# Optimization experiments

Measured on AMD Instinct MI355X. Metric: run time of the kernel, lower is better.

Reference implementation:

```python
import jax, jax.numpy as jnp
import numpy as np

NUM_SECTORS = 11


def setup_inputs() -> dict:
    key = jax.random.key(0)
    k0, k1, k2, k3 = jax.random.split(key, 4)
    B, N, C, H = 4, 2048, 512, 8
    x = jax.random.normal(k0, (B, N, C), dtype=jnp.float32)
    w_qkv = jax.random.normal(k1, (C, 3 * C), dtype=jnp.float32) * 0.02
    w_proj = jax.random.normal(k2, (C, C), dtype=jnp.float32) * 0.02
    b_proj = jnp.zeros((C,), dtype=jnp.float32)
    gate_logit = jnp.full((H,), 2.0, dtype=jnp.float32)
    sector_ids = jax.random.randint(k3, (N,), 0, NUM_SECTORS, dtype=jnp.int64)
    return {"x": x, "w_qkv": w_qkv, "w_proj": w_proj, "b_proj": b_proj,
            "gate_logit": gate_logit, "sector_ids": sector_ids}


def reference(x, w_qkv, w_proj, b_proj, gate_logit, sector_ids):
    B, N, C = x.shape
    H = gate_logit.shape[0]
    d = C // H
    scale = d ** -0.5

    qkv = (x @ w_qkv).reshape(B, N, 3, H, d)
    qkv = jnp.transpose(qkv, (2, 0, 3, 1, 4))  # (3, B, H, N, d)
    q, k, v = qkv[0], qkv[1], qkv[2]

    # Content attention: softmax(QK^T / sqrt(d)) @ V
    attn = jnp.einsum('bhnd,bhmd->bhnm', q, k) * scale
    attn = jax.nn.softmax(attn, axis=-1)
    v_content = jnp.einsum('bhnm,bhmd->bhnd', attn, v)

    # Positional path: A_pos @ V == per-sector mean of V, gathered per row.
    # A_pos[i,j] = 1/|sector(i)| if sector(i)==sector(j); row_sum >= 1 always.
    ids = sector_ids.astype(jnp.int32)
    counts = jax.ops.segment_sum(jnp.ones((N,), x.dtype), ids, num_segments=NUM_SECTORS)
    counts = jnp.maximum(counts, 1.0)
    v_nfirst = jnp.transpose(v, (2, 0, 1, 3)).reshape(N, B * H * d)  # (N, BHd)
    sums = jax.ops.segment_sum(v_nfirst, ids, num_segments=NUM_SECTORS)  # (S, BHd)
    means = sums / counts[:, None]
    v_pos = means[ids].reshape(N, B, H, d).transpose(1, 2, 0, 3)  # (B, H, N, d)

    g = jax.nn.sigmoid(gate_logit)[None, :, None, None]
    out = g * v_pos + (1.0 - g) * v_content  # (B, H, N, d)
    out = jnp.transpose(out, (0, 2, 1, 3)).reshape(B, N, C)
    return out @ w_proj + b_proj
```

## Files before the change

### kernel.cpp

```cpp
#include <hip/hip_runtime.h>
#include <hip/hip_bf16.h>
#include <stdint.h>

typedef float f32x4 __attribute__((ext_vector_type(4)));
typedef float f32x16 __attribute__((ext_vector_type(16)));
typedef short bf16x8 __attribute__((ext_vector_type(8)));
typedef short short4v __attribute__((ext_vector_type(4)));
typedef int i32x4 __attribute__((ext_vector_type(4)));

#define MFMA16(a, b, c) __builtin_amdgcn_mfma_f32_16x16x32_bf16(a, b, c, 0, 0, 0)
#define MFMA32(a, b, c) __builtin_amdgcn_mfma_f32_32x32x16_bf16(a, b, c, 0, 0, 0)

__device__ __forceinline__ float bf2f(unsigned short u) {
    unsigned int x = ((unsigned int)u) << 16;
    float f;
    __builtin_memcpy(&f, &x, 4);
    return f;
}
__device__ __forceinline__ unsigned short f2bf(float f) {
    unsigned int x;
    __builtin_memcpy(&x, &f, 4);
    unsigned int r = x + 0x7FFFu + ((x >> 16) & 1u);
    return (unsigned short)(r >> 16);
}
__device__ __forceinline__ unsigned int cvt_pk_bf16(float lo, float hi) {
    unsigned int d;
    asm("v_cvt_pk_bf16_f32 %0, %1, %2" : "=v"(d) : "v"(lo), "v"(hi));
    return d;
}

#define GLD16(g, l)                                                        \
    __builtin_amdgcn_global_load_lds(                                      \
        (const __attribute__((address_space(1))) void*)(g),                \
        (__attribute__((address_space(3))) void*)(l), 16, 0, 0)

#define QSCALE 0.18033688011112042f

__global__ __launch_bounds__(256) void k_cvt_x(const float* __restrict__ x,
                                               unsigned short* __restrict__ xb) {
    int i = (blockIdx.x * 256 + threadIdx.x) * 4;
    float4 v = *(const float4*)(x + i);
    short4v o;
    o.x = (short)f2bf(v.x);
    o.y = (short)f2bf(v.y);
    o.z = (short)f2bf(v.z);
    o.w = (short)f2bf(v.w);
    *(short4v*)(xb + i) = o;
}

__global__ __launch_bounds__(256) void k_transpose_bf16(const float* __restrict__ in,
                                                        unsigned short* __restrict__ out,
                                                        int R, int C) {
    __shared__ float tile[32][33];
    int tx = threadIdx.x & 31, ty = threadIdx.x >> 5;
    int r0 = blockIdx.y * 32, c0 = blockIdx.x * 32;
#pragma unroll
    for (int i = 0; i < 32; i += 8) tile[ty + i][tx] = in[(r0 + ty + i) * C + c0 + tx];
    __syncthreads();
#pragma unroll
    for (int i = 0; i < 32; i += 8) out[(c0 + ty + i) * R + r0 + tx] = f2bf(tile[tx][ty + i]);
}

__global__ __launch_bounds__(256) void k_gemm_qkv(const unsigned short* __restrict__ A,
                                                  const unsigned short* __restrict__ Bt,
                                                  unsigned short* __restrict__ Q,
                                                  unsigned short* __restrict__ Kd,
                                                  unsigned short* __restrict__ Vr) {
    __shared__ alignas(16) unsigned short As[128 * 64];
    __shared__ alignas(16) unsigned short Bs[128 * 64];
    const int t = threadIdx.x;
    const int w = t >> 6, l = t & 63;
    const int brow = blockIdx.x * 128, bcol = blockIdx.y * 128;
    const int wr = (w >> 1) * 64, wc = (w & 1) * 64;
    const int li = l & 15, lk = (l >> 4) * 8;
    f32x4 acc[4][4] = {};

    for (int kt = 0; kt < 512; kt += 64) {
#pragma unroll
        for (int i = 0; i < 4; i++) {
            int ub = i * 256 + w * 64;
            int r = (ub >> 3) + (l >> 3);
            int ck = l & 7;
            GLD16(A + (brow + r) * 512 + kt + ck * 8, As + ub * 8);
            GLD16(Bt + (bcol + r) * 512 + kt + ck * 8, Bs + ub * 8);
        }
        __syncthreads();
#pragma unroll
        for (int ks = 0; ks < 2; ks++) {
            bf16x8 af[4], bfr[4];
#pragma unroll
            for (int m = 0; m < 4; m++)
                af[m] = *(const bf16x8*)(As + (wr + m * 16 + li) * 64 + ks * 32 + lk);
#pragma unroll
            for (int n = 0; n < 4; n++)
                bfr[n] = *(const bf16x8*)(Bs + (wc + n * 16 + li) * 64 + ks * 32 + lk);
#pragma unroll
            for (int m = 0; m < 4; m++)
#pragma unroll
                for (int n = 0; n < 4; n++)
                    acc[m][n] = MFMA16(af[m], bfr[n], acc[m][n]);
        }
        __syncthreads();
    }
#pragma unroll
    for (int m = 0; m < 4; m++) {
#pragma unroll
        for (int n = 0; n < 4; n++) {
#pragma unroll
            for (int r = 0; r < 4; r++) {
                int gm = brow + wr + m * 16 + (l >> 4) * 4 + r;
                int gn = bcol + wc + n * 16 + li;
                float v = acc[m][n][r];
                int bb = gm >> 11, tok = gm & 2047;
                int three = gn >> 9, hh = (gn >> 6) & 7, dd = gn & 63;
                int bh = bb * 8 + hh;
                if (three == 0)
                    Q[((bh << 11) + tok) * 64 + dd] = f2bf(v * QSCALE);
                else if (three == 1)
                    Kd[((bh << 11) + tok) * 64 + dd] = f2bf(v);
                else
                    Vr[((bh << 11) + tok) * 64 + dd] = f2bf(v);
            }
        }
    }
}

__global__ __launch_bounds__(256) void k_transpose_v(const unsigned short* __restrict__ Vr,
                                                     unsigned short* __restrict__ Vt) {
    __shared__ unsigned short tile[64][68];
    int bh = blockIdx.x >> 5, nt = blockIdx.x & 31;
    int t = threadIdx.x;
    const unsigned short* src = Vr + ((size_t)bh * 2048 + nt * 64) * 64;
#pragma unroll
    for (int i = 0; i < 2; i++) {
        int row = i * 32 + (t >> 3);
        int col = (t & 7) * 8;
        *(bf16x8*)&tile[row][col] = *(const bf16x8*)(src + row * 64 + col);
    }
    __syncthreads();
    unsigned short* dst = Vt + (size_t)bh * 64 * 2048 + nt * 64;
#pragma unroll
    for (int i = 0; i < 2; i++) {
        int drow = i * 32 + (t >> 3);
        int ncol = (t & 7) * 8;
        bf16x8 v;
#pragma unroll
        for (int e = 0; e < 8; e++) v[e] = (short)tile[ncol + e][drow];
        *(bf16x8*)(dst + (size_t)drow * 2048 + ncol) = v;
    }
}

__global__ __launch_bounds__(128, 2) void k_attn(const unsigned short* __restrict__ Q,
                                                 const unsigned short* __restrict__ K,
                                                 const unsigned short* __restrict__ Vt,
                                                 float* __restrict__ vc) {
    __shared__ alignas(16) unsigned short Ks[2][64 * 64];
    __shared__ alignas(16) unsigned short Vs[2][64 * 64];
    const int bid = blockIdx.x;
    const int bh = bid >> 5, qb = bid & 31;
    const int w = threadIdx.x >> 6, l = threadIdx.x & 63;
    const int q = l & 31, hi = l >> 5;
    const unsigned short* Qh = Q + (size_t)bh * 2048 * 64;
    const char* Kb = (const char*)(K + (size_t)bh * 2048 * 64);
    const char* Vb = (const char*)(Vt + (size_t)bh * 64 * 2048);
    const int qbase = qb * 64 + w * 32;
    const int swz = (q & 7) << 4;

    bf16x8 qf[4];
#pragma unroll
    for (int ks = 0; ks < 4; ks++)
        qf[ks] = *(const bf16x8*)(Qh + (qbase + q) * 64 + ks * 16 + hi * 8);

    f32x16 o0 = {}, o1 = {};
    float mx = -1e30f, sm = 0.f;

    auto stage = [&](int buf, int kt) {
#pragma unroll
        for (int i = 0; i < 4; i++) {
            int abase = (w * 4 + i) * 1024;
            int al = abase + l * 16;
            int g = al ^ (((al >> 7) & 7) << 4);
            GLD16(Kb + (size_t)kt * 128 + g, (char*)Ks[buf] + abase);
        }
#pragma unroll
        for (int i = 0; i < 4; i++) {
            int abase = (w * 4 + i) * 1024;
            int al = abase + l * 16;
            int row = al >> 7;
            int col = (al & 127) ^ ((row & 7) << 4);
            GLD16(Vb + (size_t)row * 4096 + kt * 2 + col, (char*)Vs[buf] + abase);
        }
    };

    stage(0, 0);
    __syncthreads();

    for (int it = 0; it < 32; ++it) {
        const int cur = it & 1;
        if (it < 31) stage(cur ^ 1, (it + 1) * 64);

        const char* Kc = (const char*)Ks[cur];
        f32x16 s0 = {}, s1 = {};
        __builtin_amdgcn_s_setprio(1);
#pragma unroll
        for (int ks = 0; ks < 4; ks++) {
            bf16x8 kf0 = *(const bf16x8*)(Kc + q * 128 + ((ks * 32 + hi * 16) ^ swz));
            bf16x8 kf1 = *(const bf16x8*)(Kc + (q + 32) * 128 + ((ks * 32 + hi * 16) ^ swz));
            s0 = MFMA32(kf0, qf[ks], s0);
            s1 = MFMA32(kf1, qf[ks], s1);
        }
        __builtin_amdgcn_s_setprio(0);

        float tm = s0[0];
#pragma unroll
        for (int r = 1; r < 16; r++) tm = fmaxf(tm, s0[r]);
#pragma unroll
        for (int r = 0; r < 16; r++) tm = fmaxf(tm, s1[r]);
        tm = fmaxf(tm, __shfl_xor(tm, 32));
        float mn = fmaxf(mx, tm);
        float fac = __builtin_amdgcn_exp2f(mx - mn);
        mx = mn;
#pragma unroll
        for (int r = 0; r < 16; r++) {
            o0[r] *= fac;
            o1[r] *= fac;
        }
        float a = 0.f;
#pragma unroll
        for (int r = 0; r < 16; r++) {
            float p = __builtin_amdgcn_exp2f(s0[r] - mx);
            s0[r] = p;
            a += p;
        }
#pragma unroll
        for (int r = 0; r < 16; r++) {
            float p = __builtin_amdgcn_exp2f(s1[r] - mx);
            s1[r] = p;
            a += p;
        }
        a += __shfl_xor(a, 32);
        sm = sm * fac + a;

        unsigned int pk0[4][2], pk1[4][2], sw0[4][2], sw1[4][2];
#pragma unroll
        for (int aa = 0; aa < 4; aa++)
#pragma unroll
            for (int c = 0; c < 2; c++) {
                pk0[aa][c] = cvt_pk_bf16(s0[4 * aa + 2 * c], s0[4 * aa + 2 * c + 1]);
                pk1[aa][c] = cvt_pk_bf16(s1[4 * aa + 2 * c], s1[4 * aa + 2 * c + 1]);
            }
#pragma unroll
        for (int aa = 0; aa < 4; aa++)
#pragma unroll
            for (int c = 0; c < 2; c++) {
                sw0[aa][c] = __shfl_xor((int)pk0[aa][c], 32);
                sw1[aa][c] = __shfl_xor((int)pk1[aa][c], 32);
            }

        const char* Vc = (const char*)Vs[cur];
        __builtin_amdgcn_s_setprio(1);
#pragma unroll
        for (int ks = 0; ks < 4; ks++) {
            const int aa = ks & 1;
            unsigned int u0, u1, u2, u3;
            if (ks < 2) {
                u0 = hi ? sw0[2 * aa + 1][0] : pk0[2 * aa][0];
                u1 = hi ? sw0[2 * aa + 1][1] : pk0[2 * aa][1];
                u2 = hi ? pk0[2 * aa + 1][0] : sw0[2 * aa][0];
                u3 = hi ? pk0[2 * aa + 1][1] : sw0[2 * aa][1];
            } else {
                u0 = hi ? sw1[2 * aa + 1][0] : pk1[2 * aa][0];
                u1 = hi ? sw1[2 * aa + 1][1] : pk1[2 * aa][1];
                u2 = hi ? pk1[2 * aa + 1][0] : sw1[2 * aa][0];
                u3 = hi ? pk1[2 * aa + 1][1] : sw1[2 * aa][1];
            }
            i32x4 uu = {(int)u0, (int)u1, (int)u2, (int)u3};
            bf16x8 pa = __builtin_bit_cast(bf16x8, uu);
            bf16x8 vf0 = *(const bf16x8*)(Vc + q * 128 + ((ks * 32 + hi * 16) ^ swz));
            bf16x8 vf1 = *(const bf16x8*)(Vc + (q + 32) * 128 + ((ks * 32 + hi * 16) ^ swz));
            o0 = MFMA32(pa, vf0, o0);
            o1 = MFMA32(pa, vf1, o1);
        }
        __builtin_amdgcn_s_setprio(0);

        __syncthreads();
    }

    float inv = 1.f / sm;
    float* vout = vc + ((size_t)bh * 2048 + qbase) * 64;
#pragma unroll
    for (int r = 0; r < 16; r++) {
        int qq = (r & 3) + 8 * (r >> 2) + 4 * hi;
        float iv = __shfl(inv, qq);
        vout[qq * 64 + q] = o0[r] * iv;
        vout[qq * 64 + q + 32] = o1[r] * iv;
    }
}

__global__ void k_counts(const int* __restrict__ ids, float* __restrict__ counts) {
    int t = threadIdx.x;
    for (int n = t; n < 2048; n += 256) atomicAdd(&counts[ids[n]], 1.0f);
}

__global__ __launch_bounds__(256) void k_sums(const unsigned short* __restrict__ Vt,
                                              const int* __restrict__ ids,
                                              float* __restrict__ sums) {
    __shared__ int ids_s[512];
    int bh = blockIdx.x, ch = blockIdx.y;
    int t = threadIdx.x;
    ids_s[t] = ids[ch * 512 + t];
    ids_s[t + 256] = ids[ch * 512 + 256 + t];
    __syncthreads();
    int dd = t & 63, sub = t >> 6;
    const unsigned short* row = Vt + ((size_t)(bh * 64 + dd) << 11) + ch * 512 + sub * 128;
    const int* idp = ids_s + sub * 128;
    float acc[11] = {};
    for (int i = 0; i < 128; i++) {
        float v = bf2f(row[i]);
        int s = idp[i];
#pragma unroll
        for (int si = 0; si < 11; si++) acc[si] += (s == si) ? v : 0.f;
    }
#pragma unroll
    for (int si = 0; si < 11; si++) atomicAdd(&sums[((si * 32 + bh) << 6) + dd], acc[si]);
}

__global__ __launch_bounds__(256) void k_mix(const float* __restrict__ vc,
                                             const float* __restrict__ sums,
                                             const float* __restrict__ counts,
                                             const int* __restrict__ ids,
                                             const float* __restrict__ gate,
                                             unsigned short* __restrict__ mixb) {
    int tid = blockIdx.x * 256 + threadIdx.x;
    int m = tid >> 7;
    int c4 = (tid & 127) << 2;
    int b = m >> 11, tok = m & 2047;
    int h = c4 >> 6, dd = c4 & 63;
    int bh = b * 8 + h;
    int sid = ids[tok];
    float invc = 1.f / fmaxf(counts[sid], 1.f);
    float g = 1.f / (1.f + __expf(-gate[h]));
    float4 vp = *(const float4*)(sums + ((sid * 32 + bh) << 6) + dd);
    float4 vcv = *(const float4*)(vc + ((size_t)(bh << 11) + tok) * 64 + dd);
    short4v ov;
    ov.x = (short)f2bf(g * vp.x * invc + (1.f - g) * vcv.x);
    ov.y = (short)f2bf(g * vp.y * invc + (1.f - g) * vcv.y);
    ov.z = (short)f2bf(g * vp.z * invc + (1.f - g) * vcv.z);
    ov.w = (short)f2bf(g * vp.w * invc + (1.f - g) * vcv.w);
    *(short4v*)(mixb + (size_t)m * 512 + c4) = ov;
}

__global__ __launch_bounds__(256) void k_gemm_out(const unsigned short* __restrict__ A,
                                                  const unsigned short* __restrict__ Bt,
                                                  const float* __restrict__ bias,
                                                  float* __restrict__ out) {
    __shared__ alignas(16) unsigned short As[128 * 64];
    __shared__ alignas(16) unsigned short Bs[128 * 64];
    const int t = threadIdx.x;
    const int w = t >> 6, l = t & 63;
    const int brow = blockIdx.x * 128, bcol = blockIdx.y * 128;
    const int wr = (w >> 1) * 64, wc = (w & 1) * 64;
    const int li = l & 15, lk = (l >> 4) * 8;
    f32x4 acc[4][4] = {};

    for (int kt = 0; kt < 512; kt += 64) {
#pragma unroll
        for (int i = 0; i < 4; i++) {
            int ub = i * 256 + w * 64;
            int r = (ub >> 3) + (l >> 3);
            int ck = l & 7;
            GLD16(A + (brow + r) * 512 + kt + ck * 8, As + ub * 8);
            GLD16(Bt + (bcol + r) * 512 + kt + ck * 8, Bs + ub * 8);
        }
        __syncthreads();
#pragma unroll
        for (int ks = 0; ks < 2; ks++) {
            bf16x8 af[4], bfr[4];
#pragma unroll
            for (int m = 0; m < 4; m++)
                af[m] = *(const bf16x8*)(As + (wr + m * 16 + li) * 64 + ks * 32 + lk);
#pragma unroll
            for (int n = 0; n < 4; n++)
                bfr[n] = *(const bf16x8*)(Bs + (wc + n * 16 + li) * 64 + ks * 32 + lk);
#pragma unroll
            for (int m = 0; m < 4; m++)
#pragma unroll
                for (int n = 0; n < 4; n++)
                    acc[m][n] = MFMA16(af[m], bfr[n], acc[m][n]);
        }
        __syncthreads();
    }
#pragma unroll
    for (int m = 0; m < 4; m++) {
#pragma unroll
        for (int n = 0; n < 4; n++) {
#pragma unroll
            for (int r = 0; r < 4; r++) {
                int gm = brow + wr + m * 16 + (l >> 4) * 4 + r;
                int gn = bcol + wc + n * 16 + li;
                out[(size_t)gm * 512 + gn] = acc[m][n][r] + bias[gn];
            }
        }
    }
}

extern "C" void kernel_launch(void* const* d_in, const int* in_sizes, int n_in,
                              void* d_out, int out_size, void* d_ws, size_t ws_size,
                              hipStream_t stream) {
    const float* x = (const float*)d_in[0];
    const float* w_qkv = (const float*)d_in[1];
    const float* w_proj = (const float*)d_in[2];
    const float* b_proj = (const float*)d_in[3];
    const float* gate = (const float*)d_in[4];
    const int* ids = (const int*)d_in[5];
    float* out = (float*)d_out;
    char* ws = (char*)d_ws;

    unsigned short* xb = (unsigned short*)(ws + 0);
    unsigned short* wqT = (unsigned short*)(ws + 8388608);
    unsigned short* wpT = (unsigned short*)(ws + 9961472);
    unsigned short* Q = (unsigned short*)(ws + 10485760);
    unsigned short* Kd = (unsigned short*)(ws + 18874368);
    unsigned short* Vt = (unsigned short*)(ws + 27262976);
    float* vc = (float*)(ws + 35651584);
    unsigned short* Vrow = (unsigned short*)(ws + 35651584);
    float* sums = (float*)(ws + 52428800);
    float* counts = (float*)(ws + 52518912);
    unsigned short* mixb = xb;

    hipMemsetAsync(ws + 52428800, 0, 90112 + 64, stream);

    k_cvt_x<<<4096, 256, 0, stream>>>(x, xb);
    {
        dim3 g(48, 16);
        k_transpose_bf16<<<g, 256, 0, stream>>>(w_qkv, wqT, 512, 1536);
    }
    {
        dim3 g(16, 16);
        k_transpose_bf16<<<g, 256, 0, stream>>>(w_proj, wpT, 512, 512);
    }
    {
        dim3 g(64, 12);
        k_gemm_qkv<<<g, 256, 0, stream>>>(xb, wqT, Q, Kd, Vrow);
    }
    k_transpose_v<<<1024, 256, 0, stream>>>(Vrow, Vt);
    k_attn<<<1024, 128, 0, stream>>>(Q, Kd, Vt, vc);
    k_counts<<<1, 256, 0, stream>>>(ids, counts);
    {
        dim3 g(32, 4);
        k_sums<<<g, 256, 0, stream>>>(Vt, ids, sums);
    }
    k_mix<<<4096, 256, 0, stream>>>(vc, sums, counts, ids, gate, mixb);
    {
        dim3 g(64, 4);
        k_gemm_out<<<g, 256, 0, stream>>>(mixb, wpT, b_proj, out);
    }
}
```

Measured before the change: 228.4 us.

## Split attention key tiles across wave pairs with LDS softmax merge

The attention kernel now launches 256 threads per block, and each pair of waves shares one 32-query slice. Each wave of a pair processes half of every 64-key tile, and at the end the two partial softmax states (max, sum, output) are merged through shared memory. This doubles the wave count per block to improve latency hiding, halves per-wave register use, and restructures the max/sum reductions into shorter dependency chains. The counts kernel also accumulates into a shared-memory histogram before writing global counts. The cost is an extra merge step with a barrier, plus redundant rescaling work in each wave.

After: 215.8 us. -5.5%, faster.

```diff
diff --git a/kernel.cpp b/kernel.cpp
--- a/kernel.cpp
+++ b/kernel.cpp
@@ -150,7 +150,7 @@
     }
 }
 
-__global__ __launch_bounds__(128, 2) void k_attn(const unsigned short* __restrict__ Q,
+__global__ __launch_bounds__(256, 4) void k_attn(const unsigned short* __restrict__ Q,
                                                  const unsigned short* __restrict__ K,
                                                  const unsigned short* __restrict__ Vt,
                                                  float* __restrict__ vc) {
@@ -159,11 +159,12 @@
     const int bid = blockIdx.x;
     const int bh = bid >> 5, qb = bid & 31;
     const int w = threadIdx.x >> 6, l = threadIdx.x & 63;
+    const int wq = w >> 1, wk = w & 1;
     const int q = l & 31, hi = l >> 5;
     const unsigned short* Qh = Q + (size_t)bh * 2048 * 64;
     const char* Kb = (const char*)(K + (size_t)bh * 2048 * 64);
     const char* Vb = (const char*)(Vt + (size_t)bh * 64 * 2048);
-    const int qbase = qb * 64 + w * 32;
+    const int qbase = qb * 64 + wq * 32;
     const int swz = (q & 7) << 4;
 
     bf16x8 qf[4];
@@ -177,18 +178,19 @@
     auto stage = [&](int buf, int kt) {
 #pragma unroll
         for (int i = 0; i < 4; i++) {
-            int abase = (w * 4 + i) * 1024;
-            int al = abase + l * 16;
-            int g = al ^ (((al >> 7) & 7) << 4);
-            GLD16(Kb + (size_t)kt * 128 + g, (char*)Ks[buf] + abase);
-        }
-#pragma unroll
-        for (int i = 0; i < 4; i++) {
-            int abase = (w * 4 + i) * 1024;
-            int al = abase + l * 16;
-            int row = al >> 7;
-            int col = (al & 127) ^ ((row & 7) << 4);
-            GLD16(Vb + (size_t)row * 4096 + kt * 2 + col, (char*)Vs[buf] + abase);
+            int idx = w * 4 + i;
+            if (idx < 8) {
+                int abase = idx * 1024;
+                int al = abase + l * 16;
+                int g = al ^ (((al >> 7) & 7) << 4);
+                GLD16(Kb + (size_t)kt * 128 + g, (char*)Ks[buf] + abase);
+            } else {
+                int abase = (idx - 8) * 1024;
+                int al = abase + l * 16;
+                int row = al >> 7;
+                int col = (al & 127) ^ ((row & 7) << 4);
+                GLD16(Vb + (size_t)row * 4096 + kt * 2 + col, (char*)Vs[buf] + abase);
+            }
         }
     };
 
@@ -200,22 +202,21 @@
         if (it < 31) stage(cur ^ 1, (it + 1) * 64);
 
         const char* Kc = (const char*)Ks[cur];
-        f32x16 s0 = {}, s1 = {};
+        f32x16 s0 = {};
         __builtin_amdgcn_s_setprio(1);
 #pragma unroll
         for (int ks = 0; ks < 4; ks++) {
-            bf16x8 kf0 = *(const bf16x8*)(Kc + q * 128 + ((ks * 32 + hi * 16) ^ swz));
-            bf16x8 kf1 = *(const bf16x8*)(Kc + (q + 32) * 128 + ((ks * 32 + hi * 16) ^ swz));
-            s0 = MFMA32(kf0, qf[ks], s0);
-            s1 = MFMA32(kf1, qf[ks], s1);
+            bf16x8 kf = *(const bf16x8*)(Kc + (wk * 32 + q) * 128 + ((ks * 32 + hi * 16) ^ swz));
+            s0 = MFMA32(kf, qf[ks], s0);
         }
         __builtin_amdgcn_s_setprio(0);
 
-        float tm = s0[0];
-#pragma unroll
-        for (int r = 1; r < 16; r++) tm = fmaxf(tm, s0[r]);
-#pragma unroll
-        for (int r = 0; r < 16; r++) tm = fmaxf(tm, s1[r]);
+        float c8[8];
+#pragma unroll
+        for (int r = 0; r < 8; r++) c8[r] = fmaxf(s0[r], s0[r + 8]);
+#pragma unroll
+        for (int r = 0; r < 4; r++) c8[r] = fmaxf(c8[r], c8[r + 4]);
+        float tm = fmaxf(fmaxf(c8[0], c8[1]), fmaxf(c8[2], c8[3]));
         tm = fmaxf(tm, __shfl_xor(tm, 32));
         float mn = fmaxf(mx, tm);
         float fac = __builtin_amdgcn_exp2f(mx - mn);
@@ -225,59 +226,50 @@
             o0[r] *= fac;
             o1[r] *= fac;
         }
-        float a = 0.f;
-#pragma unroll
-        for (int r = 0; r < 16; r++) {
-            float p = __builtin_amdgcn_exp2f(s0[r] - mx);
-            s0[r] = p;
-            a += p;
-        }
-#pragma unroll
-        for (int r = 0; r < 16; r++) {
-            float p = __builtin_amdgcn_exp2f(s1[r] - mx);
-            s1[r] = p;
-            a += p;
-        }
+        float a0 = 0.f, a1 = 0.f, a2 = 0.f, a3 = 0.f;
+#pragma unroll
+        for (int r = 0; r < 16; r += 4) {
+            float p0 = __builtin_amdgcn_exp2f(s0[r] - mx);
+            float p1 = __builtin_amdgcn_exp2f(s0[r + 1] - mx);
+            float p2 = __builtin_amdgcn_exp2f(s0[r + 2] - mx);
+            float p3 = __builtin_amdgcn_exp2f(s0[r + 3] - mx);
+            s0[r] = p0;
+            s0[r + 1] = p1;
+            s0[r + 2] = p2;
+            s0[r + 3] = p3;
+            a0 += p0;
+            a1 += p1;
+            a2 += p2;
+            a3 += p3;
+        }
+        float a = (a0 + a1) + (a2 + a3);
         a += __shfl_xor(a, 32);
         sm = sm * fac + a;
 
-        unsigned int pk0[4][2], pk1[4][2], sw0[4][2], sw1[4][2];
+        unsigned int pk[4][2];
 #pragma unroll
         for (int aa = 0; aa < 4; aa++)
 #pragma unroll
-            for (int c = 0; c < 2; c++) {
-                pk0[aa][c] = cvt_pk_bf16(s0[4 * aa + 2 * c], s0[4 * aa + 2 * c + 1]);
-                pk1[aa][c] = cvt_pk_bf16(s1[4 * aa + 2 * c], s1[4 * aa + 2 * c + 1]);
-            }
-#pragma unroll
-        for (int aa = 0; aa < 4; aa++)
-#pragma unroll
-            for (int c = 0; c < 2; c++) {
-                sw0[aa][c] = __shfl_xor((int)pk0[aa][c], 32);
-                sw1[aa][c] = __shfl_xor((int)pk1[aa][c], 32);
-            }
+            for (int c = 0; c < 2; c++)
+                pk[aa][c] = cvt_pk_bf16(s0[4 * aa + 2 * c], s0[4 * aa + 2 * c + 1]);
 
         const char* Vc = (const char*)Vs[cur];
         __builtin_amdgcn_s_setprio(1);
 #pragma unroll
-        for (int ks = 0; ks < 4; ks++) {
-            const int aa = ks & 1;
-            unsigned int u0, u1, u2, u3;
-            if (ks < 2) {
-                u0 = hi ? sw0[2 * aa + 1][0] : pk0[2 * aa][0];
-                u1 = hi ? sw0[2 * aa + 1][1] : pk0[2 * aa][1];
-                u2 = hi ? pk0[2 * aa + 1][0] : sw0[2 * aa][0];
-                u3 = hi ? pk0[2 * aa + 1][1] : sw0[2 * aa][1];
-            } else {
-                u0 = hi ? sw1[2 * aa + 1][0] : pk1[2 * aa][0];
-                u1 = hi ? sw1[2 * aa + 1][1] : pk1[2 * aa][1];
-                u2 = hi ? pk1[2 * aa + 1][0] : sw1[2 * aa][0];
-                u3 = hi ? pk1[2 * aa + 1][1] : sw1[2 * aa][1];
-            }
+        for (int ksl = 0; ksl < 2; ksl++) {
+            unsigned int send0 = hi ? pk[2 * ksl][0] : pk[2 * ksl + 1][0];
+            unsigned int send1 = hi ? pk[2 * ksl][1] : pk[2 * ksl + 1][1];
+            unsigned int r0 = (unsigned int)__shfl_xor((int)send0, 32);
+            unsigned int r1 = (unsigned int)__shfl_xor((int)send1, 32);
+            unsigned int u0 = hi ? r0 : pk[2 * ksl][0];
+            unsigned int u1 = hi ? r1 : pk[2 * ksl][1];
+            unsigned int u2 = hi ? pk[2 * ksl + 1][0] : r0;
+            unsigned int u3 = hi ? pk[2 * ksl + 1][1] : r1;
             i32x4 uu = {(int)u0, (int)u1, (int)u2, (int)u3};
             bf16x8 pa = __builtin_bit_cast(bf16x8, uu);
-            bf16x8 vf0 = *(const bf16x8*)(Vc + q * 128 + ((ks * 32 + hi * 16) ^ swz));
-            bf16x8 vf1 = *(const bf16x8*)(Vc + (q + 32) * 128 + ((ks * 32 + hi * 16) ^ swz));
+            int vcol = (wk * 64 + ksl * 32 + hi * 16);
+            bf16x8 vf0 = *(const bf16x8*)(Vc + q * 128 + (vcol ^ swz));
+            bf16x8 vf1 = *(const bf16x8*)(Vc + (q + 32) * 128 + (vcol ^ swz));
             o0 = MFMA32(pa, vf0, o0);
             o1 = MFMA32(pa, vf1, o1);
         }
@@ -286,20 +278,45 @@
         __syncthreads();
     }
 
-    float inv = 1.f / sm;
-    float* vout = vc + ((size_t)bh * 2048 + qbase) * 64;
-#pragma unroll
-    for (int r = 0; r < 16; r++) {
-        int qq = (r & 3) + 8 * (r >> 2) + 4 * hi;
-        float iv = __shfl(inv, qq);
-        vout[qq * 64 + q] = o0[r] * iv;
-        vout[qq * 64 + q + 32] = o1[r] * iv;
+    float* So = ((float*)Ks) + wq * 2048;
+    float* Sml = ((float*)Vs) + wq * 128;
+    if (wk == 1) {
+#pragma unroll
+        for (int r = 0; r < 16; r++) {
+            So[r * 64 + l] = o0[r];
+            So[(16 + r) * 64 + l] = o1[r];
+        }
+        Sml[l] = mx;
+        Sml[64 + l] = sm;
+    }
+    __syncthreads();
+    if (wk == 0) {
+        float m1 = Sml[l], l1 = Sml[64 + l];
+        float ms = fmaxf(mx, m1);
+        float f0 = __builtin_amdgcn_exp2f(mx - ms);
+        float f1 = __builtin_amdgcn_exp2f(m1 - ms);
+        float inv = 1.f / (f0 * sm + f1 * l1);
+        float* vout = vc + ((size_t)bh * 2048 + qbase) * 64;
+#pragma unroll
+        for (int r = 0; r < 16; r++) {
+            float om0 = f0 * o0[r] + f1 * So[r * 64 + l];
+            float om1 = f0 * o1[r] + f1 * So[(16 + r) * 64 + l];
+            int qq = (r & 3) + 8 * (r >> 2) + 4 * hi;
+            float iv = __shfl(inv, qq);
+            vout[qq * 64 + q] = om0 * iv;
+            vout[qq * 64 + q + 32] = om1 * iv;
+        }
     }
 }
 
 __global__ void k_counts(const int* __restrict__ ids, float* __restrict__ counts) {
+    __shared__ float h[11];
     int t = threadIdx.x;
-    for (int n = t; n < 2048; n += 256) atomicAdd(&counts[ids[n]], 1.0f);
+    if (t < 11) h[t] = 0.f;
+    __syncthreads();
+    for (int n = t; n < 2048; n += 256) atomicAdd(&h[ids[n]], 1.0f);
+    __syncthreads();
+    if (t < 11) counts[t] = h[t];
 }
 
 __global__ __launch_bounds__(256) void k_sums(const unsigned short* __restrict__ Vt,
@@ -444,7 +461,7 @@
         k_gemm_qkv<<<g, 256, 0, stream>>>(xb, wqT, Q, Kd, Vrow);
     }
     k_transpose_v<<<1024, 256, 0, stream>>>(Vrow, Vt);
-    k_attn<<<1024, 128, 0, stream>>>(Q, Kd, Vt, vc);
+    k_attn<<<1024, 256, 0, stream>>>(Q, Kd, Vt, vc);
     k_counts<<<1, 256, 0, stream>>>(ids, counts);
     {
         dim3 g(32, 4);
```
